# Kernel optimization log

Hardware: AMD Instinct MI355X
Metric: run time of the kernel (lower is better)

The kernel has to match this reference:

```python
import jax, jax.numpy as jnp
import numpy as np

H_SIZE = 1024
N_HEADS = 16
HEAD_DIM = H_SIZE // N_HEADS
TAU2 = 1.0
LN_EPS = 1e-5


def setup_inputs() -> dict:
    key = jax.random.key(0)
    ks = jax.random.split(key, 12)
    B, S = 2, 1024
    s = 1.0 / np.sqrt(H_SIZE)
    inp = {
        "input": jax.random.normal(ks[0], (B, S, H_SIZE), dtype=jnp.float32),
        "input_mask": jnp.ones((B, S), dtype=jnp.float32),
        # uniform(0,1) noise; converted to Gumbel(0,1) inside reference
        "gumbel": jax.random.uniform(ks[1], (B, N_HEADS, S, S), dtype=jnp.float32,
                                     minval=1e-10, maxval=1.0),
        "Wq": jax.random.normal(ks[2], (H_SIZE, H_SIZE), dtype=jnp.float32) * s,
        "bq": jnp.zeros((H_SIZE,), dtype=jnp.float32),
        "Wk": jax.random.normal(ks[3], (H_SIZE, H_SIZE), dtype=jnp.float32) * s,
        "bk": jnp.zeros((H_SIZE,), dtype=jnp.float32),
        "Wv": jax.random.normal(ks[4], (H_SIZE, H_SIZE), dtype=jnp.float32) * s,
        "bv": jnp.zeros((H_SIZE,), dtype=jnp.float32),
        "Wo": jax.random.normal(ks[5], (H_SIZE, H_SIZE), dtype=jnp.float32) * s,
        "bo": jnp.zeros((H_SIZE,), dtype=jnp.float32),
        "gamma": jnp.ones((H_SIZE,), dtype=jnp.float32),
        "beta": jnp.zeros((H_SIZE,), dtype=jnp.float32),
    }
    return inp


def reference(input, input_mask, gumbel, Wq, bq, Wk, bk, Wv, bv, Wo, bo, gamma, beta):
    B, S, _ = input.shape
    # projections -> [B, H, S, D]
    def proj(W, b):
        y = jnp.einsum('bsh,oh->bso', input, W) + b  # torch Linear: x @ W.T + b
        return y.reshape(B, S, N_HEADS, HEAD_DIM).transpose(0, 2, 1, 3)
    qq = proj(Wq, bq)
    kk = proj(Wk, bk)
    vv = proj(Wv, bv)
    # raw scores (NOTE: original has no 1/sqrt(d) scaling)
    interact = jnp.einsum('bhqd,bhkd->bhqk', qq, kk)
    # gumbel-softmax (soft): softmax((logits + g)/tau)
    g = -jnp.log(-jnp.log(gumbel))
    sto_attn = jax.nn.softmax((interact + g) / TAU2, axis=-1)
    # masking: mask_1 over query dim, mask_2 over key dim
    mask = input_mask[:, None, :, None] * input_mask[:, None, None, :]  # [B,1,S,S]
    attn = sto_attn * mask
    # (dropout p=0 -> identity)
    out = jnp.einsum('bhqk,bhkd->bhqd', attn, vv)
    out = out.transpose(0, 2, 1, 3).reshape(B, S, H_SIZE)
    out = jnp.einsum('bsh,oh->bso', out, Wo) + bo
    # residual + layernorm
    x = out + input
    mu = jnp.mean(x, axis=-1, keepdims=True)
    var = jnp.mean(jnp.square(x - mu), axis=-1, keepdims=True)
    return (x - mu) * jax.lax.rsqrt(var + LN_EPS) * gamma + beta
```

## Files before the change

kernel.cpp:

```cpp
#include <hip/hip_runtime.h>

#define S_LEN 1024
#define HSZ   1024
#define NHEAD 16
#define HD    64
#define BATCH 2
#define MROWS 2048
#define SOFTMAX_M0 50.0f

typedef unsigned short u16;
typedef __attribute__((ext_vector_type(8))) short short8;
typedef __attribute__((ext_vector_type(4))) short short4v;
typedef __attribute__((ext_vector_type(4))) float f32x4;

#define MFMA_BF16(a, b, c) __builtin_amdgcn_mfma_f32_16x16x32_bf16((a), (b), (c), 0, 0, 0)

__device__ __forceinline__ u16 f2bf(float f) {
    union { float f; unsigned u; } c; c.f = f;
    unsigned u = c.u;
    u += 0x7fffu + ((u >> 16) & 1u);
    return (u16)(u >> 16);
}
__device__ __forceinline__ float bf2f(u16 s) {
    union { unsigned u; float f; } c; c.u = ((unsigned)s) << 16;
    return c.f;
}
__device__ __forceinline__ short8 ld8(const u16* p) {
    return *reinterpret_cast<const short8*>(p);
}
__device__ __forceinline__ void gld16(const u16* g, u16* l) {
    __builtin_amdgcn_global_load_lds(
        (const __attribute__((address_space(1))) unsigned int*)g,
        (__attribute__((address_space(3))) unsigned int*)l, 16, 0, 0);
}
__device__ __forceinline__ int frag_off(int row, int cbb) {
    return (((row << 3) | (cbb ^ (row & 7))) << 3);
}

template<int MT>
__device__ __forceinline__ void gemm_tile(const u16* __restrict__ Ag,
                                          const u16* __restrict__ Bg,
                                          int klen, u16* As, u16* Bs,
                                          f32x4 (&acc)[MT][4]) {
    const int tid  = threadIdx.x;
    const int wave = tid >> 6, lane = tid & 63;
    const int lr = lane & 15, grp = lane >> 4;
    const int wm = wave >> 1, wn = wave & 1;

#pragma unroll
    for (int mt = 0; mt < MT; mt++)
#pragma unroll
        for (int nt = 0; nt < 4; nt++)
            acc[mt][nt] = (f32x4){0.f, 0.f, 0.f, 0.f};

    for (int k0 = 0; k0 < klen; k0 += 64) {
        __syncthreads();
#pragma unroll
        for (int j = 0; j < MT; j++) {
            int c = j * 256 + tid, row = c >> 3, cb = (c & 7) ^ (row & 7);
            gld16(Ag + (size_t)row * HSZ + k0 + cb * 8, As + c * 8);
        }
#pragma unroll
        for (int j = 0; j < 4; j++) {
            int c = j * 256 + tid, row = c >> 3, cb = (c & 7) ^ (row & 7);
            gld16(Bg + (size_t)row * HSZ + k0 + cb * 8, Bs + c * 8);
        }
        __syncthreads();

#pragma unroll
        for (int h = 0; h < 2; h++) {
            const int cbb = h * 4 + grp;
            short8 af[MT], bf[4];
#pragma unroll
            for (int mt = 0; mt < MT; mt++)
                af[mt] = ld8(As + frag_off(wm * (MT * 16) + mt * 16 + lr, cbb));
#pragma unroll
            for (int nt = 0; nt < 4; nt++)
                bf[nt] = ld8(Bs + frag_off(wn * 64 + nt * 16 + lr, cbb));
#pragma unroll
            for (int mt = 0; mt < MT; mt++)
#pragma unroll
                for (int nt = 0; nt < 4; nt++)
                    acc[mt][nt] = MFMA_BF16(af[mt], bf[nt], acc[mt][nt]);
        }
    }
}

__global__ __launch_bounds__(256)
void convert_kernel(const float* __restrict__ x,  const float* __restrict__ wq,
                    const float* __restrict__ wk, const float* __restrict__ wv,
                    const float* __restrict__ wo, u16* __restrict__ dst) {
    const int XV = (MROWS * HSZ) / 4;
    const int WV = (HSZ * HSZ) / 4;
    int vid = blockIdx.x * 256 + threadIdx.x;
    const float* src; int off;
    if (vid < XV)            { src = x;  off = vid; }
    else if (vid < XV + WV)  { src = wq; off = vid - XV; }
    else if (vid < XV + 2*WV){ src = wk; off = vid - XV - WV; }
    else if (vid < XV + 3*WV){ src = wv; off = vid - XV - 2*WV; }
    else                     { src = wo; off = vid - XV - 3*WV; }
    float4 v = reinterpret_cast<const float4*>(src)[off];
    ushort4 o;
    o.x = f2bf(v.x); o.y = f2bf(v.y); o.z = f2bf(v.z); o.w = f2bf(v.w);
    reinterpret_cast<ushort4*>(dst)[vid] = o;
}

__global__ __launch_bounds__(256)
void qkv_gemm(const u16* __restrict__ xb,
              const u16* __restrict__ wqb, const u16* __restrict__ wkb,
              const u16* __restrict__ wvb,
              const float* __restrict__ bq, const float* __restrict__ bk,
              const float* __restrict__ bv, const float* __restrict__ mask,
              u16* __restrict__ qout, u16* __restrict__ kout,
              u16* __restrict__ vtout) {
    __shared__ u16 As[64 * 64];
    __shared__ u16 Bs[128 * 64];
    const int ntile = blockIdx.x;
    const int mtile = blockIdx.y;
    const int p  = ntile >> 3;
    const int m0 = mtile * 64;
    const int nw = (ntile & 7) * 128;
    const u16*  W    = (p == 0) ? wqb : (p == 1) ? wkb : wvb;
    const float* bias = (p == 0) ? bq : (p == 1) ? bk : bv;

    f32x4 acc[2][4];
    gemm_tile<2>(xb + (size_t)m0 * HSZ, W + (size_t)nw * HSZ, HSZ, As, Bs, acc);

    const int wave = threadIdx.x >> 6, lane = threadIdx.x & 63;
    const int lr = lane & 15, grp = lane >> 4;
    const int wm = wave >> 1, wn = wave & 1;
#pragma unroll
    for (int mt = 0; mt < 2; mt++)
#pragma unroll
        for (int nt = 0; nt < 4; nt++)
#pragma unroll
            for (int r = 0; r < 4; r++) {
                int m = m0 + wm * 32 + mt * 16 + grp * 4 + r;
                int o = nw + wn * 64 + nt * 16 + lr;
                float val = acc[mt][nt][r] + bias[o];
                int b = m >> 10, s = m & 1023, hh = o >> 6, d = o & 63;
                if (p == 0)
                    qout[(((size_t)(b * NHEAD + hh)) * S_LEN + s) * HD + d] = f2bf(val);
                else if (p == 1)
                    kout[(((size_t)(b * NHEAD + hh)) * S_LEN + s) * HD + d] = f2bf(val);
                else
                    vtout[(((size_t)(b * NHEAD + hh)) * HD + d) * S_LEN + s] =
                        f2bf(val * mask[m]);
            }
}

__global__ __launch_bounds__(256, 4)
void attn_kernel(const u16* __restrict__ qb, const u16* __restrict__ kb,
                 const u16* __restrict__ vt, const float* __restrict__ gumbel,
                 u16* __restrict__ po, float* __restrict__ pl) {
    const int bh   = blockIdx.y;
    const int qt   = blockIdx.x;
    const int half = blockIdx.z;
    const int q0 = qt * 64, kbase = half * 512;
    const int tid = threadIdx.x;
    const int wave = tid >> 6, lane = tid & 63;
    const int lr = lane & 15, grp = lane >> 4;

    const u16* Q = qb + (size_t)bh * S_LEN * HD;
    const u16* K = kb + (size_t)bh * S_LEN * HD;
    const u16* V = vt + (size_t)bh * HD * S_LEN;
    const float* G = gumbel + (size_t)bh * S_LEN * S_LEN;
    const int qw = q0 + wave * 16;

    __shared__ u16 Ks[64 * 64];
    __shared__ u16 Vs[64 * 64];
    __shared__ u16 pbuf[4 * 16 * 68];

    u16* pw = pbuf + wave * (16 * 68);

    short8 aq0 = ld8(Q + (size_t)(qw + lr) * HD + grp * 8);
    short8 aq1 = ld8(Q + (size_t)(qw + lr) * HD + 32 + grp * 8);

    f32x4 acco[4];
#pragma unroll
    for (int i = 0; i < 4; i++) acco[i] = (f32x4){0.f, 0.f, 0.f, 0.f};
    float lsum[4] = {0.f, 0.f, 0.f, 0.f};

    const float* Grow[4];
#pragma unroll
    for (int r = 0; r < 4; r++)
        Grow[r] = G + (size_t)(qw + grp * 4 + r) * S_LEN + lr;

    for (int it = 0; it < 8; it++) {
        const int k0 = kbase + it * 64;
        __syncthreads();
#pragma unroll
        for (int j = 0; j < 2; j++) {
            int c = j * 256 + tid, row = c >> 3, cb = (c & 7) ^ (row & 7);
            gld16(K + (size_t)(k0 + row) * HD + cb * 8, Ks + c * 8);
        }
#pragma unroll
        for (int j = 0; j < 2; j++) {
            int c = j * 256 + tid, row = c >> 3, cb = (c & 7) ^ (row & 7);
            gld16(V + (size_t)row * S_LEN + k0 + cb * 8, Vs + c * 8);
        }
        float w[4][4];
#pragma unroll
        for (int kt = 0; kt < 4; kt++)
#pragma unroll
            for (int r = 0; r < 4; r++) {
                float u = Grow[r][k0 + kt * 16];
                w[kt][r] = -__builtin_amdgcn_rcpf(__logf(u));
            }
        __syncthreads();

        float sc[4][4];
#pragma unroll
        for (int kt = 0; kt < 4; kt++) {
            int row = kt * 16 + lr;
            f32x4 a = (f32x4){0.f, 0.f, 0.f, 0.f};
            a = MFMA_BF16(aq0, ld8(Ks + frag_off(row, grp)), a);
            a = MFMA_BF16(aq1, ld8(Ks + frag_off(row, 4 + grp)), a);
#pragma unroll
            for (int r = 0; r < 4; r++) sc[kt][r] = a[r];
        }

#pragma unroll
        for (int kt = 0; kt < 4; kt++)
#pragma unroll
            for (int r = 0; r < 4; r++) {
                float p = __expf(sc[kt][r] - SOFTMAX_M0) * w[kt][r];
                lsum[r] += p;
                pw[(grp * 4 + r) * 68 + kt * 16 + lr] = f2bf(p);
            }

        short8 pa[2];
#pragma unroll
        for (int ks = 0; ks < 2; ks++) {
            const u16* pp = pw + lr * 68 + ks * 32 + grp * 8;
            short4v lo = *reinterpret_cast<const short4v*>(pp);
            short4v hi = *reinterpret_cast<const short4v*>(pp + 4);
            pa[ks] = __builtin_shufflevector(lo, hi, 0, 1, 2, 3, 4, 5, 6, 7);
        }

#pragma unroll
        for (int nt = 0; nt < 4; nt++) {
            int row = nt * 16 + lr;
#pragma unroll
            for (int ks = 0; ks < 2; ks++)
                acco[nt] = MFMA_BF16(pa[ks], ld8(Vs + frag_off(row, ks * 4 + grp)),
                                     acco[nt]);
        }
    }

#pragma unroll
    for (int r = 0; r < 4; r++) {
        float s = lsum[r];
#pragma unroll
        for (int off = 1; off < 16; off <<= 1)
            s += __shfl_xor(s, off, 64);
        lsum[r] = s;
    }

    const int qidx = ((half * 32 + bh) * 16 + qt) * 64 + wave * 16 + grp * 4;
    if (lr == 0) {
#pragma unroll
        for (int r = 0; r < 4; r++) pl[qidx + r] = lsum[r];
    }
#pragma unroll
    for (int nt = 0; nt < 4; nt++)
#pragma unroll
        for (int r = 0; r < 4; r++)
            po[(size_t)(qidx + r) * 64 + nt * 16 + lr] = f2bf(acco[nt][r]);
}

__global__ __launch_bounds__(256)
void combine_kernel(const u16* __restrict__ po, const float* __restrict__ pl,
                    const float* __restrict__ mask, u16* __restrict__ ctx) {
    const int qt = blockIdx.x, bh = blockIdx.y;
    const int b = bh >> 4, h = bh & 15;
    const int q = threadIdx.x >> 2;
    const int dc = (threadIdx.x & 3) * 16;
    const int i0 = ((0 * 32 + bh) * 16 + qt) * 64 + q;
    const int i1 = ((1 * 32 + bh) * 16 + qt) * 64 + q;
    float l = pl[i0] + pl[i1];
    float mq = mask[b * S_LEN + qt * 64 + q] / l;
    u16* dst = ctx + ((size_t)(b * S_LEN + qt * 64 + q)) * HSZ + h * 64 + dc;
#pragma unroll
    for (int c = 0; c < 2; c++) {
        short8 a = ld8(po + (size_t)i0 * 64 + dc + c * 8);
        short8 bm = ld8(po + (size_t)i1 * 64 + dc + c * 8);
        short8 o;
#pragma unroll
        for (int j = 0; j < 8; j++)
            o[j] = (short)f2bf((bf2f((u16)a[j]) + bf2f((u16)bm[j])) * mq);
        *reinterpret_cast<short8*>(dst + c * 8) = o;
    }
}

__global__ __launch_bounds__(256)
void oproj_gemm(const u16* __restrict__ A, const u16* __restrict__ W,
                float* __restrict__ part0, float* __restrict__ part1) {
    __shared__ u16 As[64 * 64];
    __shared__ u16 Bs[128 * 64];
    const int ntile = blockIdx.x;
    const int mtile = blockIdx.y;
    const int z     = blockIdx.z;
    const int m0 = mtile * 64, n0 = ntile * 128, koff = z * 512;

    f32x4 acc[2][4];
    gemm_tile<2>(A + (size_t)m0 * HSZ + koff, W + (size_t)n0 * HSZ + koff,
                 512, As, Bs, acc);

    float* dst = z ? part1 : part0;
    const int wave = threadIdx.x >> 6, lane = threadIdx.x & 63;
    const int lr = lane & 15, grp = lane >> 4;
    const int wm = wave >> 1, wn = wave & 1;
#pragma unroll
    for (int mt = 0; mt < 2; mt++)
#pragma unroll
        for (int nt = 0; nt < 4; nt++)
#pragma unroll
            for (int r = 0; r < 4; r++) {
                int m = m0 + wm * 32 + mt * 16 + grp * 4 + r;
                int o = n0 + wn * 64 + nt * 16 + lr;
                dst[(size_t)m * HSZ + o] = acc[mt][nt][r];
            }
}

__global__ __launch_bounds__(256)
void ln_kernel(const float* __restrict__ part0, const float* __restrict__ part1,
               const float* __restrict__ xin, const float* __restrict__ bo,
               const float* __restrict__ gamma, const float* __restrict__ beta,
               float* __restrict__ out) {
    const int row = blockIdx.x;
    const int tid = threadIdx.x;
    const size_t base = (size_t)row * (HSZ / 4);

    float4 p0 = reinterpret_cast<const float4*>(part0)[base + tid];
    float4 p1 = reinterpret_cast<const float4*>(part1)[base + tid];
    float4 xr = reinterpret_cast<const float4*>(xin)[base + tid];
    float4 bb = reinterpret_cast<const float4*>(bo)[tid];
    float4 v;
    v.x = p0.x + p1.x + xr.x + bb.x;
    v.y = p0.y + p1.y + xr.y + bb.y;
    v.z = p0.z + p1.z + xr.z + bb.z;
    v.w = p0.w + p1.w + xr.w + bb.w;

    float s  = v.x + v.y + v.z + v.w;
    float ss = v.x * v.x + v.y * v.y + v.z * v.z + v.w * v.w;
#pragma unroll
    for (int off = 1; off < 64; off <<= 1) {
        s  += __shfl_xor(s, off, 64);
        ss += __shfl_xor(ss, off, 64);
    }
    __shared__ float red[8];
    int wave = tid >> 6, lane = tid & 63;
    if (lane == 0) { red[wave] = s; red[4 + wave] = ss; }
    __syncthreads();
    s  = red[0] + red[1] + red[2] + red[3];
    ss = red[4] + red[5] + red[6] + red[7];
    float mu  = s * (1.f / HSZ);
    float var = ss * (1.f / HSZ) - mu * mu;
    float rstd = rsqrtf(var + 1e-5f);

    float4 g  = reinterpret_cast<const float4*>(gamma)[tid];
    float4 be = reinterpret_cast<const float4*>(beta)[tid];
    float4 o;
    o.x = (v.x - mu) * rstd * g.x + be.x;
    o.y = (v.y - mu) * rstd * g.y + be.y;
    o.z = (v.z - mu) * rstd * g.z + be.z;
    o.w = (v.w - mu) * rstd * g.w + be.w;
    reinterpret_cast<float4*>(out)[base + tid] = o;
}

extern "C" void kernel_launch(void* const* d_in, const int* in_sizes, int n_in,
                              void* d_out, int out_size, void* d_ws, size_t ws_size,
                              hipStream_t stream) {
    (void)in_sizes; (void)n_in; (void)out_size; (void)ws_size;
    const float* x     = (const float*)d_in[0];
    const float* mask  = (const float*)d_in[1];
    const float* gum   = (const float*)d_in[2];
    const float* Wq    = (const float*)d_in[3];
    const float* bq    = (const float*)d_in[4];
    const float* Wk    = (const float*)d_in[5];
    const float* bk    = (const float*)d_in[6];
    const float* Wv    = (const float*)d_in[7];
    const float* bv    = (const float*)d_in[8];
    const float* Wo    = (const float*)d_in[9];
    const float* bo    = (const float*)d_in[10];
    const float* gamma = (const float*)d_in[11];
    const float* beta  = (const float*)d_in[12];
    float* out = (float*)d_out;

    u16* xb  = (u16*)d_ws;
    u16* wqb = xb  + 2097152;
    u16* wkb = wqb + 1048576;
    u16* wvb = wkb + 1048576;
    u16* wob = wvb + 1048576;
    u16* qb  = wob + 1048576;
    u16* kb  = qb  + 2097152;
    u16* vt  = kb  + 2097152;
    u16* ctx = vt  + 2097152;
    float* part0 = (float*)(ctx + 2097152);
    float* pl    = (float*)((char*)part0 + 8388608);
    u16*   po    = xb;
    float* part1 = (float*)xb;

    convert_kernel<<<dim3(6144), dim3(256), 0, stream>>>(x, Wq, Wk, Wv, Wo, xb);
    qkv_gemm<<<dim3(24, 32), dim3(256), 0, stream>>>(xb, wqb, wkb, wvb,
                                                     bq, bk, bv, mask,
                                                     qb, kb, vt);
    attn_kernel<<<dim3(16, 32, 2), dim3(256), 0, stream>>>(qb, kb, vt, gum, po, pl);
    combine_kernel<<<dim3(16, 32), dim3(256), 0, stream>>>(po, pl, mask, ctx);
    oproj_gemm<<<dim3(8, 32, 2), dim3(256), 0, stream>>>(ctx, wob, part0, part1);
    ln_kernel<<<dim3(2048), dim3(256), 0, stream>>>(part0, part1, x, bo,
                                                    gamma, beta, out);
}
```

Measured before the change: 288.8 us.

## Widen GEMM K-tile to 128, prefetch gumbel, compute row sums via MFMA

The shared GEMM tile loop now stages 128-wide K slices with a 16-way XOR swizzle, which halves the number of barrier-separated iterations but doubles LDS use per block. In the attention kernel, the gumbel noise for the next key tile is loaded one iteration ahead, and the log/reciprocal and exp now use the hardware log2/exp2 builtins with the offset folded into constants. Softmax row sums are taken from an MFMA against a vector of bf16 ones instead of scalar accumulation plus shuffle reductions. As a side effect, the sums are now computed from the bf16-rounded probabilities, which changes numerics slightly.

```diff
diff --git a/kernel.cpp b/kernel.cpp
--- a/kernel.cpp
+++ b/kernel.cpp
@@ -6,7 +6,8 @@
 #define HD    64
 #define BATCH 2
 #define MROWS 2048
-#define SOFTMAX_M0 50.0f
+#define LOG2E 1.4426950408889634f
+#define M0L2  72.134752044448f
 
 typedef unsigned short u16;
 typedef __attribute__((ext_vector_type(8))) short short8;
@@ -35,6 +36,9 @@
 }
 __device__ __forceinline__ int frag_off(int row, int cbb) {
     return (((row << 3) | (cbb ^ (row & 7))) << 3);
+}
+__device__ __forceinline__ int frag_off16(int row, int cbb) {
+    return (((row << 4) | (cbb ^ (row & 15))) << 3);
 }
 
 template<int MT>
@@ -53,30 +57,30 @@
         for (int nt = 0; nt < 4; nt++)
             acc[mt][nt] = (f32x4){0.f, 0.f, 0.f, 0.f};
 
-    for (int k0 = 0; k0 < klen; k0 += 64) {
+    for (int k0 = 0; k0 < klen; k0 += 128) {
         __syncthreads();
 #pragma unroll
-        for (int j = 0; j < MT; j++) {
-            int c = j * 256 + tid, row = c >> 3, cb = (c & 7) ^ (row & 7);
+        for (int j = 0; j < 2 * MT; j++) {
+            int c = j * 256 + tid, row = c >> 4, cb = (c & 15) ^ (row & 15);
             gld16(Ag + (size_t)row * HSZ + k0 + cb * 8, As + c * 8);
         }
 #pragma unroll
-        for (int j = 0; j < 4; j++) {
-            int c = j * 256 + tid, row = c >> 3, cb = (c & 7) ^ (row & 7);
+        for (int j = 0; j < 8; j++) {
+            int c = j * 256 + tid, row = c >> 4, cb = (c & 15) ^ (row & 15);
             gld16(Bg + (size_t)row * HSZ + k0 + cb * 8, Bs + c * 8);
         }
         __syncthreads();
 
 #pragma unroll
-        for (int h = 0; h < 2; h++) {
+        for (int h = 0; h < 4; h++) {
             const int cbb = h * 4 + grp;
             short8 af[MT], bf[4];
 #pragma unroll
             for (int mt = 0; mt < MT; mt++)
-                af[mt] = ld8(As + frag_off(wm * (MT * 16) + mt * 16 + lr, cbb));
+                af[mt] = ld8(As + frag_off16(wm * (MT * 16) + mt * 16 + lr, cbb));
 #pragma unroll
             for (int nt = 0; nt < 4; nt++)
-                bf[nt] = ld8(Bs + frag_off(wn * 64 + nt * 16 + lr, cbb));
+                bf[nt] = ld8(Bs + frag_off16(wn * 64 + nt * 16 + lr, cbb));
 #pragma unroll
             for (int mt = 0; mt < MT; mt++)
 #pragma unroll
@@ -113,8 +117,8 @@
               const float* __restrict__ bv, const float* __restrict__ mask,
               u16* __restrict__ qout, u16* __restrict__ kout,
               u16* __restrict__ vtout) {
-    __shared__ u16 As[64 * 64];
-    __shared__ u16 Bs[128 * 64];
+    __shared__ u16 As[64 * 128];
+    __shared__ u16 Bs[128 * 128];
     const int ntile = blockIdx.x;
     const int mtile = blockIdx.y;
     const int p  = ntile >> 3;
@@ -176,15 +180,26 @@
     short8 aq0 = ld8(Q + (size_t)(qw + lr) * HD + grp * 8);
     short8 aq1 = ld8(Q + (size_t)(qw + lr) * HD + 32 + grp * 8);
 
+    short8 ones;
+#pragma unroll
+    for (int j = 0; j < 8; j++) ones[j] = (short)0x3F80;
+
     f32x4 acco[4];
 #pragma unroll
     for (int i = 0; i < 4; i++) acco[i] = (f32x4){0.f, 0.f, 0.f, 0.f};
-    float lsum[4] = {0.f, 0.f, 0.f, 0.f};
+    f32x4 accl = (f32x4){0.f, 0.f, 0.f, 0.f};
 
     const float* Grow[4];
 #pragma unroll
     for (int r = 0; r < 4; r++)
         Grow[r] = G + (size_t)(qw + grp * 4 + r) * S_LEN + lr;
+
+    float gpre[4][4];
+#pragma unroll
+    for (int kt = 0; kt < 4; kt++)
+#pragma unroll
+        for (int r = 0; r < 4; r++)
+            gpre[kt][r] = Grow[r][kbase + kt * 16];
 
     for (int it = 0; it < 8; it++) {
         const int k0 = kbase + it * 64;
@@ -203,11 +218,17 @@
 #pragma unroll
         for (int kt = 0; kt < 4; kt++)
 #pragma unroll
-            for (int r = 0; r < 4; r++) {
-                float u = Grow[r][k0 + kt * 16];
-                w[kt][r] = -__builtin_amdgcn_rcpf(__logf(u));
-            }
+            for (int r = 0; r < 4; r++)
+                w[kt][r] = __builtin_amdgcn_rcpf(__builtin_amdgcn_logf(gpre[kt][r]));
         __syncthreads();
+
+        if (it < 7) {
+#pragma unroll
+            for (int kt = 0; kt < 4; kt++)
+#pragma unroll
+                for (int r = 0; r < 4; r++)
+                    gpre[kt][r] = Grow[r][k0 + 64 + kt * 16];
+        }
 
         float sc[4][4];
 #pragma unroll
@@ -224,9 +245,8 @@
         for (int kt = 0; kt < 4; kt++)
 #pragma unroll
             for (int r = 0; r < 4; r++) {
-                float p = __expf(sc[kt][r] - SOFTMAX_M0) * w[kt][r];
-                lsum[r] += p;
-                pw[(grp * 4 + r) * 68 + kt * 16 + lr] = f2bf(p);
+                float e = __builtin_amdgcn_exp2f(fmaf(sc[kt][r], LOG2E, -M0L2));
+                pw[(grp * 4 + r) * 68 + kt * 16 + lr] = f2bf(e * w[kt][r]);
             }
 
         short8 pa[2];
@@ -246,21 +266,15 @@
                 acco[nt] = MFMA_BF16(pa[ks], ld8(Vs + frag_off(row, ks * 4 + grp)),
                                      acco[nt]);
         }
-    }
-
-#pragma unroll
-    for (int r = 0; r < 4; r++) {
-        float s = lsum[r];
-#pragma unroll
-        for (int off = 1; off < 16; off <<= 1)
-            s += __shfl_xor(s, off, 64);
-        lsum[r] = s;
+#pragma unroll
+        for (int ks = 0; ks < 2; ks++)
+            accl = MFMA_BF16(pa[ks], ones, accl);
     }
 
     const int qidx = ((half * 32 + bh) * 16 + qt) * 64 + wave * 16 + grp * 4;
     if (lr == 0) {
 #pragma unroll
-        for (int r = 0; r < 4; r++) pl[qidx + r] = lsum[r];
+        for (int r = 0; r < 4; r++) pl[qidx + r] = accl[r];
     }
 #pragma unroll
     for (int nt = 0; nt < 4; nt++)
@@ -296,8 +310,8 @@
 __global__ __launch_bounds__(256)
 void oproj_gemm(const u16* __restrict__ A, const u16* __restrict__ W,
                 float* __restrict__ part0, float* __restrict__ part1) {
-    __shared__ u16 As[64 * 64];
-    __shared__ u16 Bs[128 * 64];
+    __shared__ u16 As[64 * 128];
+    __shared__ u16 Bs[128 * 128];
     const int ntile = blockIdx.x;
     const int mtile = blockIdx.y;
     const int z     = blockIdx.z;
```

New measurement: 289.0 us. No clear change (+0.1%).
